# Kernel optimization log

Hardware: AMD Instinct MI355X
Metric: run time of the kernel (lower is better)

## Reference

```python
import jax, jax.numpy as jnp
import numpy as np

B, N, D, H, QK, FF, E, K = 32, 400, 128, 8, 16, 512, 8, 2
LOSS_COEF = 1e-2


def layer_norm(x, g, b, eps=1e-5):
    m = x.mean(-1, keepdims=True)
    v = ((x - m) ** 2).mean(-1, keepdims=True)
    return (x - m) / jnp.sqrt(v + eps) * g + b


def cv_sq(x, eps=1e-10):
    return x.var() / (x.mean() ** 2 + eps)


def setup_inputs() -> dict:
    key = jax.random.key(0)
    ks = jax.random.split(key, 10)
    w = lambda i, shape: jax.random.normal(ks[i], shape, jnp.float32) * 0.02
    return {
        "x": jax.random.normal(ks[0], (B, N, D), jnp.float32),
        "Wq": w(1, (D, H * QK)),
        "Wk": w(2, (D, H * QK)),
        "Wv": w(3, (D, H * QK)),
        "Wo": w(4, (H * QK, D)),
        "bo": jnp.zeros((D,), jnp.float32),
        "ln1_g": jnp.ones((D,), jnp.float32),
        "ln1_b": jnp.zeros((D,), jnp.float32),
        "w_gate": w(5, (D, E)),
        "W1": w(6, (E, D, FF)),
        "b1": jnp.zeros((E, FF), jnp.float32),
        "W2": w(7, (E, FF, D)),
        "b2": jnp.zeros((E, D), jnp.float32),
        "ln2_g": jnp.ones((D,), jnp.float32),
        "ln2_b": jnp.zeros((D,), jnp.float32),
    }


def reference(x, Wq, Wk, Wv, Wo, bo, ln1_g, ln1_b, w_gate, W1, b1, W2, b2, ln2_g, ln2_b):
    b, n, d = x.shape
    # multi-head self-attention (no mask in encoder)
    q = (x @ Wq).reshape(b, n, H, QK).transpose(0, 2, 1, 3)  # [b,h,n,qk]
    k = (x @ Wk).reshape(b, n, H, QK).transpose(0, 2, 1, 3)
    v = (x @ Wv).reshape(b, n, H, QK).transpose(0, 2, 1, 3)
    score = jnp.einsum("bhnd,bhmd->bhnm", q, k) / (QK ** 0.5)
    weights = jax.nn.softmax(score, axis=-1)
    out = jnp.einsum("bhnm,bhmd->bhnd", weights, v)
    out_concat = out.transpose(0, 2, 1, 3).reshape(b, n, H * QK)
    mh = out_concat @ Wo + bo
    out1 = layer_norm(x + mh, ln1_g, ln1_b)

    # MoE feed-forward: noisy top-k gating in eval mode (clean logits)
    xf = out1.reshape(-1, d)                       # [T, D]
    T = xf.shape[0]
    logits = xf @ w_gate                           # [T, E]
    top_vals, top_idx = jax.lax.top_k(logits, K)   # [T, K]
    top_gates = jax.nn.softmax(top_vals, axis=-1)
    gates = jnp.zeros((T, E), xf.dtype).at[jnp.arange(T)[:, None], top_idx].set(top_gates)
    # dense per-expert compute, sparse combine (same math as dispatch/combine)
    h = jax.nn.relu(jnp.einsum("td,edf->etf", xf, W1) + b1[:, None, :])  # [E,T,FF]
    y = jnp.einsum("etf,efd->etd", h, W2) + b2[:, None, :]               # [E,T,D]
    moe_out = jnp.einsum("etd,te->td", y, gates).reshape(b, n, d)
    importance = gates.sum(0)
    load = (gates > 0).sum(0).astype(xf.dtype)
    moe_loss = (cv_sq(importance) + cv_sq(load)) * LOSS_COEF

    out3 = layer_norm(out1 + moe_out, ln2_g, ln2_b)
    return (out3, moe_loss)
```

## Files before the change

kernel.cpp:

```cpp
#include <hip/hip_runtime.h>
#include <hip/hip_bf16.h>
#include <math.h>

#define Bb 32
#define Nn 400
#define Dd 128
#define Hh 8
#define QKd 16
#define FFd 512
#define Ee 8
#define Tt (Bb*Nn)
#define KPAD 434
#define PP2 34

typedef __attribute__((ext_vector_type(8))) __bf16 bf16x8;
typedef __attribute__((ext_vector_type(4))) float f32x4;

#if defined(__has_builtin)
#if __has_builtin(__builtin_amdgcn_exp2f)
#define EXP2(x) __builtin_amdgcn_exp2f(x)
#endif
#endif
#ifndef EXP2
#define EXP2(x) __expf((x) * 0.69314718f)
#endif

__device__ __forceinline__ unsigned short f2bfu(float f){
  union { __hip_bfloat16 h; unsigned short u; } v;
  v.h = __float2bfloat16(f);
  return v.u;
}
__device__ __forceinline__ short f2bf(float f){ return (short)f2bfu(f); }
__device__ __forceinline__ unsigned pack2bf(float a, float b){
  return (unsigned)f2bfu(a) | ((unsigned)f2bfu(b) << 16);
}
__device__ __forceinline__ bf16x8 zero_bf16x8(){
  union { uint4 u; bf16x8 b; } z;
  z.u.x = 0u; z.u.y = 0u; z.u.z = 0u; z.u.w = 0u;
  return z.b;
}

__global__ __launch_bounds__(256) void prep_kernel(
    const float* __restrict__ W1, const float* __restrict__ W2, const float* __restrict__ Wo,
    const float* __restrict__ Wq, const float* __restrict__ Wk, const float* __restrict__ Wv,
    short* __restrict__ W1t, short* __restrict__ W2t, short* __restrict__ wo_t,
    short* __restrict__ qkvw, int* __restrict__ gmeta)
{
  const int bid = blockIdx.x;
  if (bid == 0 && threadIdx.x < 24) gmeta[threadIdx.x] = 0;

  const float* in; short* out; int C, tile;
  if (bid < 512)        { int e = bid >> 6;         tile = bid & 63;          in = W1 + e*65536; out = W1t + e*65536; C = 512; }
  else if (bid < 1024)  { int e = (bid - 512) >> 6; tile = (bid - 512) & 63;  in = W2 + e*65536; out = W2t + e*65536; C = 128; }
  else if (bid < 1040)  { tile = bid - 1024; in = Wo; out = wo_t;          C = 128; }
  else if (bid < 1056)  { tile = bid - 1040; in = Wq; out = qkvw;          C = 128; }
  else if (bid < 1072)  { tile = bid - 1056; in = Wk; out = qkvw + 16384;  C = 128; }
  else                  { tile = bid - 1072; in = Wv; out = qkvw + 32768;  C = 128; }
  const int R = (bid < 512) ? 128 : (bid < 1024 ? 512 : 128);

  __shared__ float t32[32][33];
  const int nCt = C >> 5;
  const int c0 = (tile % nCt) << 5;
  const int r0 = (tile / nCt) << 5;
  const int tx = threadIdx.x & 31, ty = threadIdx.x >> 5;
  #pragma unroll
  for (int i = 0; i < 4; ++i)
    t32[ty + 8*i][tx] = in[(size_t)(r0 + ty + 8*i) * C + c0 + tx];
  __syncthreads();
  #pragma unroll
  for (int i = 0; i < 4; ++i)
    out[(size_t)(c0 + ty + 8*i) * R + r0 + tx] = f2bf(t32[tx][ty + 8*i]);
}

__global__ __launch_bounds__(256) void qkv_kernel(const float* __restrict__ x,
    const short* __restrict__ qkvw,
    short* __restrict__ q, short* __restrict__ k, short* __restrict__ v)
{
  __shared__ short xsh[64][136];
  __shared__ short xsl[64][136];
  const int tid = threadIdx.x;
  const int t0 = blockIdx.x * 64;

  #pragma unroll
  for (int it = 0; it < 8; ++it) {
    int lin = it * 256 + tid;
    int r = lin >> 5;
    int c4 = (lin & 31) << 2;
    float4 xv = *(const float4*)&x[(size_t)(t0 + r) * Dd + c4];
    unsigned h01 = pack2bf(xv.x, xv.y);
    unsigned h23 = pack2bf(xv.z, xv.w);
    union { unsigned u; float f; } ua, ub, uc, ud;
    ua.u = h01 << 16; ub.u = h01 & 0xFFFF0000u;
    uc.u = h23 << 16; ud.u = h23 & 0xFFFF0000u;
    unsigned l01 = pack2bf(xv.x - ua.f, xv.y - ub.f);
    unsigned l23 = pack2bf(xv.z - uc.f, xv.w - ud.f);
    uint2 ph; ph.x = h01; ph.y = h23;
    uint2 pl; pl.x = l01; pl.y = l23;
    *(uint2*)&xsh[r][c4] = ph;
    *(uint2*)&xsl[r][c4] = pl;
  }
  __syncthreads();

  const int lane = tid & 63, w = tid >> 6;
  const int l15 = lane & 15, l4 = lane >> 4;

  f32x4 zero4 = {0.f, 0.f, 0.f, 0.f};
  f32x4 acc[6][4];
  #pragma unroll
  for (int ot = 0; ot < 6; ++ot)
    #pragma unroll
    for (int mt = 0; mt < 4; ++mt) acc[ot][mt] = zero4;

  #pragma unroll
  for (int kt = 0; kt < 4; ++kt) {
    bf16x8 bmh[4], bml[4];
    #pragma unroll
    for (int mt = 0; mt < 4; ++mt) {
      bmh[mt] = *(const bf16x8*)&xsh[mt*16 + l15][kt*32 + l4*8];
      bml[mt] = *(const bf16x8*)&xsl[mt*16 + l15][kt*32 + l4*8];
    }
    #pragma unroll
    for (int ot = 0; ot < 6; ++ot) {
      bf16x8 a = *(const bf16x8*)&qkvw[(size_t)(w*96 + ot*16 + l15) * Dd + kt*32 + l4*8];
      #pragma unroll
      for (int mt = 0; mt < 4; ++mt) {
        acc[ot][mt] = __builtin_amdgcn_mfma_f32_16x16x32_bf16(a, bmh[mt], acc[ot][mt], 0, 0, 0);
        acc[ot][mt] = __builtin_amdgcn_mfma_f32_16x16x32_bf16(a, bml[mt], acc[ot][mt], 0, 0, 0);
      }
    }
  }

  #pragma unroll
  for (int ot = 0; ot < 6; ++ot) {
    const int ob = w*96 + ot*16;
    const int sel = ob >> 7;
    const int hz = (ob & 127) >> 4;
    #pragma unroll
    for (int mt = 0; mt < 4; ++mt) {
      int t = t0 + mt*16 + l15;
      int b = t / Nn, n = t - b * Nn;
      size_t bhn = (size_t)(b*Hh + hz) * Nn + n;
      f32x4 a = acc[ot][mt];
      uint2 p;
      if (sel == 0) {
        p.x = pack2bf(a[0]*0.36067376f, a[1]*0.36067376f);
        p.y = pack2bf(a[2]*0.36067376f, a[3]*0.36067376f);
        *(uint2*)&q[bhn*16 + l4*4] = p;
      } else if (sel == 1) {
        p.x = pack2bf(a[0], a[1]);
        p.y = pack2bf(a[2], a[3]);
        *(uint2*)&k[bhn*16 + l4*4] = p;
      } else {
        p.x = pack2bf(a[0], a[1]);
        p.y = pack2bf(a[2], a[3]);
        *(uint2*)&v[bhn*16 + l4*4] = p;
      }
    }
  }
}

__global__ __launch_bounds__(1024) void attn_kernel(const short* __restrict__ q,
    const short* __restrict__ k, const short* __restrict__ v, short* __restrict__ attn_b)
{
  __shared__ short VT[16 * KPAD];
  __shared__ short P[16][4][16 * PP2];
  const int tid = threadIdx.x;
  const int bh = blockIdx.x;

  {
    const unsigned* vg = (const unsigned*)(v + (size_t)bh * 400 * 16);
    #pragma unroll
    for (int it = 0; it < 4; ++it) {
      int lin = it*1024 + tid;
      if (lin < 3200) {
        int key = lin >> 3, dp = lin & 7;
        unsigned pv = vg[key*8 + dp];
        VT[(2*dp)  * KPAD + key] = (short)(pv & 0xffffu);
        VT[(2*dp+1)* KPAD + key] = (short)(pv >> 16);
      }
    }
    if (tid < 256) {
      int d = tid >> 4, key = 400 + (tid & 15);
      VT[d*KPAD + key] = 0;
    }
  }
  __syncthreads();

  const int w = tid >> 6, lane = tid & 63;
  const int l15 = lane & 15, g = lane >> 4;
  const int p = w & 7, hh = w >> 3;
  const int cc0 = hh ? 7 : 0;
  const int cc1 = hh ? 13 : 7;

  f32x4 zero4 = {0.f, 0.f, 0.f, 0.f};
  f32x4 o[4];
  float lsum[4];
  bf16x8 qf[4];
  #pragma unroll
  for (int i = 0; i < 4; ++i) {
    o[i] = zero4; lsum[i] = 0.f;
    int qt = p + 8*i;
    if (qt < 25 && g < 2)
      qf[i] = *(const bf16x8*)&q[((size_t)bh*400 + qt*16 + l15)*16 + 8*g];
    else
      qf[i] = zero_bf16x8();
  }

  for (int cc = cc0; cc < cc1; ++cc) {
    #pragma unroll
    for (int sub = 0; sub < 2; ++sub) {
      const int kt = cc*2 + sub;
      if (kt < 25) {
        bf16x8 kf;
        if (g < 2) kf = *(const bf16x8*)&k[((size_t)bh*400 + kt*16 + l15)*16 + 8*g];
        else       kf = zero_bf16x8();
        #pragma unroll
        for (int i = 0; i < 4; ++i) {
          int qt = p + 8*i;
          if (qt < 25) {
            f32x4 s = __builtin_amdgcn_mfma_f32_16x16x32_bf16(kf, qf[i], zero4, 0, 0, 0);
            float p0 = EXP2(s[0]);
            float p1 = EXP2(s[1]);
            float p2 = EXP2(s[2]);
            float p3 = EXP2(s[3]);
            lsum[i] += (p0 + p1) + (p2 + p3);
            uint2 pk;
            pk.x = pack2bf(p0, p1);
            pk.y = pack2bf(p2, p3);
            *(uint2*)&P[w][i][l15*PP2 + sub*16 + 4*g] = pk;
          }
        }
      } else {
        uint2 z; z.x = 0u; z.y = 0u;
        #pragma unroll
        for (int i = 0; i < 4; ++i) {
          int qt = p + 8*i;
          if (qt < 25) *(uint2*)&P[w][i][l15*PP2 + sub*16 + 4*g] = z;
        }
      }
    }
    bf16x8 vf = *(const bf16x8*)&VT[l15*KPAD + cc*32 + 8*g];
    #pragma unroll
    for (int i = 0; i < 4; ++i) {
      int qt = p + 8*i;
      if (qt < 25) {
        bf16x8 pf = *(const bf16x8*)&P[w][i][l15*PP2 + 8*g];
        o[i] = __builtin_amdgcn_mfma_f32_16x16x32_bf16(vf, pf, o[i], 0, 0, 0);
      }
    }
  }

  #pragma unroll
  for (int i = 0; i < 4; ++i) {
    lsum[i] += __shfl_xor(lsum[i], 16, 64);
    lsum[i] += __shfl_xor(lsum[i], 32, 64);
  }

  __syncthreads();
  float* CB = (float*)&P[0][0][0];
  if (hh == 1) {
    #pragma unroll
    for (int i = 0; i < 4; ++i) {
      int qt = p + 8*i;
      if (qt < 25) {
        int base = (((p*4) + i)*64 + lane)*5;
        CB[base+0] = o[i][0]; CB[base+1] = o[i][1];
        CB[base+2] = o[i][2]; CB[base+3] = o[i][3];
        CB[base+4] = lsum[i];
      }
    }
  }
  __syncthreads();
  if (hh == 0) {
    const int b = bh >> 3, h = bh & 7;
    #pragma unroll
    for (int i = 0; i < 4; ++i) {
      int qt = p + 8*i;
      if (qt < 25) {
        int base = (((p*4) + i)*64 + lane)*5;
        float o0 = o[i][0] + CB[base+0];
        float o1 = o[i][1] + CB[base+1];
        float o2 = o[i][2] + CB[base+2];
        float o3 = o[i][3] + CB[base+3];
        float ls = lsum[i] + CB[base+4];
        float inv = 1.f / ls;
        uint2 pk;
        pk.x = pack2bf(o0*inv, o1*inv);
        pk.y = pack2bf(o2*inv, o3*inv);
        *(uint2*)&attn_b[((size_t)b*Nn + qt*16 + l15)*Dd + h*16 + 4*g] = pk;
      }
    }
  }
}

__global__ __launch_bounds__(256) void proj_ln1_gate_kernel(
    const float* __restrict__ x, const short* __restrict__ attn_b,
    const short* __restrict__ wo_t, const float* __restrict__ bo,
    const float* __restrict__ g1, const float* __restrict__ b1n,
    const float* __restrict__ w_gate,
    short* __restrict__ out1b,
    int* __restrict__ cnt, float* __restrict__ imp, float* __restrict__ loadv,
    int* __restrict__ etok, float* __restrict__ egate)
{
  __shared__ short as_[64][136];
  __shared__ float reds[4][64];
  __shared__ float reds2[4][64];
  __shared__ float mv[64][2];
  __shared__ float lgs[64*8];
  __shared__ float wgs[128*8];
  __shared__ float s_imp[8], s_load[8];
  __shared__ int s_cnt[8], s_base[8];

  const int tid = threadIdx.x;
  const int t0 = blockIdx.x * 64;

  #pragma unroll
  for (int it = 0; it < 8; ++it) {
    int lin = it * 256 + tid;
    int r = lin >> 5;
    int c4 = (lin & 31) << 2;
    *(uint2*)&as_[r][c4] = *(const uint2*)&attn_b[(size_t)(t0 + r) * Dd + c4];
  }
  #pragma unroll
  for (int it = 0; it < 4; ++it) wgs[it*256 + tid] = w_gate[it*256 + tid];
  lgs[tid] = 0.f; lgs[tid + 256] = 0.f;
  if (tid < 8) { s_imp[tid] = 0.f; s_load[tid] = 0.f; s_cnt[tid] = 0; }
  __syncthreads();

  const int lane = tid & 63, w = tid >> 6;
  const int l15 = lane & 15, l4 = lane >> 4;

  f32x4 zero4 = {0.f, 0.f, 0.f, 0.f};
  f32x4 y[2][4];
  #pragma unroll
  for (int dt = 0; dt < 2; ++dt)
    #pragma unroll
    for (int mt = 0; mt < 4; ++mt) y[dt][mt] = zero4;

  #pragma unroll
  for (int kt = 0; kt < 4; ++kt) {
    bf16x8 a0 = *(const bf16x8*)&wo_t[(size_t)(w*32 + l15) * Dd + kt*32 + l4*8];
    bf16x8 a1 = *(const bf16x8*)&wo_t[(size_t)(w*32 + 16 + l15) * Dd + kt*32 + l4*8];
    bf16x8 bm[4];
    #pragma unroll
    for (int mt = 0; mt < 4; ++mt)
      bm[mt] = *(const bf16x8*)&as_[mt*16 + l15][kt*32 + l4*8];
    #pragma unroll
    for (int mt = 0; mt < 4; ++mt) {
      y[0][mt] = __builtin_amdgcn_mfma_f32_16x16x32_bf16(a0, bm[mt], y[0][mt], 0, 0, 0);
      y[1][mt] = __builtin_amdgcn_mfma_f32_16x16x32_bf16(a1, bm[mt], y[1][mt], 0, 0, 0);
    }
  }

  float4 bov[2];
  bov[0] = *(const float4*)&bo[w*32 + 0*16 + l4*4];
  bov[1] = *(const float4*)&bo[w*32 + 1*16 + l4*4];
  float sP[4], s2P[4];
  #pragma unroll
  for (int mt = 0; mt < 4; ++mt) { sP[mt] = 0.f; s2P[mt] = 0.f; }
  #pragma unroll
  for (int mt = 0; mt < 4; ++mt) {
    int row = mt*16 + l15;
    #pragma unroll
    for (int dt = 0; dt < 2; ++dt) {
      int dim = w*32 + dt*16 + l4*4;
      float4 xv = *(const float4*)&x[(size_t)(t0 + row) * Dd + dim];
      float4 bv = bov[dt];
      f32x4 r = y[dt][mt];
      r[0] += bv.x + xv.x; r[1] += bv.y + xv.y;
      r[2] += bv.z + xv.z; r[3] += bv.w + xv.w;
      y[dt][mt] = r;
      sP[mt]  += (r[0] + r[1]) + (r[2] + r[3]);
      s2P[mt] += (r[0]*r[0] + r[1]*r[1]) + (r[2]*r[2] + r[3]*r[3]);
    }
  }
  #pragma unroll
  for (int mt = 0; mt < 4; ++mt) {
    sP[mt]  += __shfl_xor(sP[mt], 16, 64);  sP[mt]  += __shfl_xor(sP[mt], 32, 64);
    s2P[mt] += __shfl_xor(s2P[mt], 16, 64); s2P[mt] += __shfl_xor(s2P[mt], 32, 64);
  }
  if (l4 == 0) {
    #pragma unroll
    for (int mt = 0; mt < 4; ++mt) {
      reds[w][mt*16 + l15] = sP[mt];
      reds2[w][mt*16 + l15] = s2P[mt];
    }
  }
  __syncthreads();
  if (tid < 64) {
    float s = reds[0][tid] + reds[1][tid] + reds[2][tid] + reds[3][tid];
    float s2 = reds2[0][tid] + reds2[1][tid] + reds2[2][tid] + reds2[3][tid];
    float m = s * (1.f/128.f);
    float var = s2 * (1.f/128.f) - m*m;
    mv[tid][0] = m;
    mv[tid][1] = rsqrtf(var + 1e-5f);
  }
  __syncthreads();

  float4 gv[2], bv2[2];
  #pragma unroll
  for (int dt = 0; dt < 2; ++dt) {
    gv[dt]  = *(const float4*)&g1[w*32 + dt*16 + l4*4];
    bv2[dt] = *(const float4*)&b1n[w*32 + dt*16 + l4*4];
  }
  #pragma unroll
  for (int mt = 0; mt < 4; ++mt) {
    int row = mt*16 + l15;
    float m = mv[row][0], inv = mv[row][1];
    float lg[8];
    #pragma unroll
    for (int e = 0; e < 8; ++e) lg[e] = 0.f;
    #pragma unroll
    for (int dt = 0; dt < 2; ++dt) {
      int dim = w*32 + dt*16 + l4*4;
      f32x4 r = y[dt][mt];
      float o0 = (r[0]-m)*inv*((float*)&gv[dt])[0] + ((float*)&bv2[dt])[0];
      float o1 = (r[1]-m)*inv*((float*)&gv[dt])[1] + ((float*)&bv2[dt])[1];
      float o2 = (r[2]-m)*inv*((float*)&gv[dt])[2] + ((float*)&bv2[dt])[2];
      float o3 = (r[3]-m)*inv*((float*)&gv[dt])[3] + ((float*)&bv2[dt])[3];
      uint2 p; p.x = pack2bf(o0, o1); p.y = pack2bf(o2, o3);
      *(uint2*)&out1b[(size_t)(t0 + row) * Dd + dim] = p;
      #pragma unroll
      for (int e = 0; e < 8; ++e)
        lg[e] += o0*wgs[(dim+0)*8+e] + o1*wgs[(dim+1)*8+e]
               + o2*wgs[(dim+2)*8+e] + o3*wgs[(dim+3)*8+e];
    }
    #pragma unroll
    for (int e = 0; e < 8; ++e) {
      lg[e] += __shfl_xor(lg[e], 16, 64);
      lg[e] += __shfl_xor(lg[e], 32, 64);
    }
    if (l4 == 0) {
      #pragma unroll
      for (int e = 0; e < 8; ++e) atomicAdd(&lgs[row*8 + e], lg[e]);
    }
  }
  __syncthreads();

  int i0 = 0, i1 = -1, p0 = 0, p1 = 0;
  float g0 = 0.f, gg1 = 0.f;
  if (tid < 64) {
    float lgv[8];
    #pragma unroll
    for (int e = 0; e < 8; ++e) lgv[e] = lgs[tid*8 + e];
    float v0 = lgv[0];
    #pragma unroll
    for (int e = 1; e < 8; ++e) if (lgv[e] > v0) { v0 = lgv[e]; i0 = e; }
    float v1 = -INFINITY;
    #pragma unroll
    for (int e = 0; e < 8; ++e) if (e != i0 && lgv[e] > v1) { v1 = lgv[e]; i1 = e; }
    g0 = 1.f / (1.f + __expf(v1 - v0));
    gg1 = 1.f - g0;
    atomicAdd(&s_imp[i0], g0);  atomicAdd(&s_imp[i1], gg1);
    atomicAdd(&s_load[i0], 1.f); atomicAdd(&s_load[i1], 1.f);
    p0 = atomicAdd(&s_cnt[i0], 1);
    p1 = atomicAdd(&s_cnt[i1], 1);
  }
  __syncthreads();
  if (tid < 8) {
    s_base[tid] = atomicAdd(&cnt[tid], s_cnt[tid]);
    atomicAdd(&imp[tid], s_imp[tid]);
    atomicAdd(&loadv[tid], s_load[tid]);
  }
  __syncthreads();
  if (tid < 64) {
    int t = t0 + tid;
    int o0 = i0 * Tt + s_base[i0] + p0;
    etok[o0] = t;               egate[o0] = g0;
    int o1 = i1 * Tt + s_base[i1] + p1;
    etok[o1] = t | (1 << 30);   egate[o1] = gg1;
  }
}

__global__ __launch_bounds__(256) void moe_kernel(const short* __restrict__ out1b,
    const short* __restrict__ W1t, const float* __restrict__ b1,
    const short* __restrict__ W2t, const float* __restrict__ b2,
    const int* __restrict__ cnt, const int* __restrict__ etok, const float* __restrict__ egate,
    short* __restrict__ moe0, short* __restrict__ moe1)
{
  __shared__ short xs[64][136];
  __shared__ short hs[64][136];
  __shared__ int els[64];
  __shared__ float gls[64];

  const int e = blockIdx.y;
  const int count = cnt[e];
  const int t0 = blockIdx.x * 64;
  if (t0 >= count) return;
  const int nt = min(64, count - t0);
  const int tid = threadIdx.x;

  if (tid < 64) {
    int idx = (tid < nt) ? tid : 0;
    els[tid] = etok[e * Tt + t0 + idx];
    gls[tid] = (tid < nt) ? egate[e * Tt + t0 + tid] : 0.f;
  }
  __syncthreads();

  #pragma unroll
  for (int it = 0; it < 8; ++it) {
    int lin = it * 256 + tid;
    int r = lin >> 5;
    int c4 = (lin & 31) << 2;
    int tok = els[r] & 0x3FFFFFFF;
    *(uint2*)&xs[r][c4] = *(const uint2*)&out1b[(size_t)tok * Dd + c4];
  }
  __syncthreads();

  const int lane = tid & 63;
  const int w = tid >> 6;
  const int l15 = lane & 15;
  const int l4 = lane >> 4;

  f32x4 zero4 = {0.f, 0.f, 0.f, 0.f};
  f32x4 y[2][4];
  #pragma unroll
  for (int dt = 0; dt < 2; ++dt)
    #pragma unroll
    for (int mt = 0; mt < 4; ++mt) y[dt][mt] = zero4;

  const short* W1p = W1t + (size_t)e * FFd * Dd;
  const short* W2p = W2t + (size_t)e * Dd * FFd;

  for (int ch = 0; ch < 4; ++ch) {
    f32x4 h[2][4];
    #pragma unroll
    for (int ft = 0; ft < 2; ++ft)
      #pragma unroll
      for (int mt = 0; mt < 4; ++mt) h[ft][mt] = zero4;

    #pragma unroll
    for (int kt = 0; kt < 4; ++kt) {
      bf16x8 a0 = *(const bf16x8*)&W1p[(size_t)(ch*128 + w*32 + 0*16 + l15) * Dd + kt*32 + l4*8];
      bf16x8 a1 = *(const bf16x8*)&W1p[(size_t)(ch*128 + w*32 + 1*16 + l15) * Dd + kt*32 + l4*8];
      bf16x8 bm[4];
      #pragma unroll
      for (int mt = 0; mt < 4; ++mt)
        bm[mt] = *(const bf16x8*)&xs[mt*16 + l15][kt*32 + l4*8];
      #pragma unroll
      for (int mt = 0; mt < 4; ++mt) {
        h[0][mt] = __builtin_amdgcn_mfma_f32_16x16x32_bf16(a0, bm[mt], h[0][mt], 0, 0, 0);
        h[1][mt] = __builtin_amdgcn_mfma_f32_16x16x32_bf16(a1, bm[mt], h[1][mt], 0, 0, 0);
      }
    }

    float4 b1v0 = *(const float4*)&b1[e*FFd + ch*128 + w*32 + 0*16 + l4*4];
    float4 b1v1 = *(const float4*)&b1[e*FFd + ch*128 + w*32 + 1*16 + l4*4];
    __syncthreads();
    #pragma unroll
    for (int mt = 0; mt < 4; ++mt) {
      uint2 p0, p1;
      p0.x = pack2bf(fmaxf(h[0][mt][0] + b1v0.x, 0.f), fmaxf(h[0][mt][1] + b1v0.y, 0.f));
      p0.y = pack2bf(fmaxf(h[0][mt][2] + b1v0.z, 0.f), fmaxf(h[0][mt][3] + b1v0.w, 0.f));
      *(uint2*)&hs[mt*16 + l15][w*32 + 0*16 + l4*4] = p0;
      p1.x = pack2bf(fmaxf(h[1][mt][0] + b1v1.x, 0.f), fmaxf(h[1][mt][1] + b1v1.y, 0.f));
      p1.y = pack2bf(fmaxf(h[1][mt][2] + b1v1.z, 0.f), fmaxf(h[1][mt][3] + b1v1.w, 0.f));
      *(uint2*)&hs[mt*16 + l15][w*32 + 1*16 + l4*4] = p1;
    }
    __syncthreads();

    #pragma unroll
    for (int kt = 0; kt < 4; ++kt) {
      bf16x8 a0 = *(const bf16x8*)&W2p[(size_t)(w*32 + 0*16 + l15) * FFd + ch*128 + kt*32 + l4*8];
      bf16x8 a1 = *(const bf16x8*)&W2p[(size_t)(w*32 + 1*16 + l15) * FFd + ch*128 + kt*32 + l4*8];
      bf16x8 bm[4];
      #pragma unroll
      for (int mt = 0; mt < 4; ++mt)
        bm[mt] = *(const bf16x8*)&hs[mt*16 + l15][kt*32 + l4*8];
      #pragma unroll
      for (int mt = 0; mt < 4; ++mt) {
        y[0][mt] = __builtin_amdgcn_mfma_f32_16x16x32_bf16(a0, bm[mt], y[0][mt], 0, 0, 0);
        y[1][mt] = __builtin_amdgcn_mfma_f32_16x16x32_bf16(a1, bm[mt], y[1][mt], 0, 0, 0);
      }
    }
  }

  float4 b2v[2];
  b2v[0] = *(const float4*)&b2[e*Dd + w*32 + 0*16 + l4*4];
  b2v[1] = *(const float4*)&b2[e*Dd + w*32 + 1*16 + l4*4];
  #pragma unroll
  for (int mt = 0; mt < 4; ++mt) {
    int m = mt*16 + l15;
    if (m < nt) {
      int raw = els[m];
      int t = raw & 0x3FFFFFFF;
      float g = gls[m];
      short* basep = (raw & (1 << 30)) ? moe1 : moe0;
      #pragma unroll
      for (int dt = 0; dt < 2; ++dt) {
        float v0 = g * (y[dt][mt][0] + ((dt == 0) ? b2v[0].x : b2v[1].x));
        float v1 = g * (y[dt][mt][1] + ((dt == 0) ? b2v[0].y : b2v[1].y));
        float v2 = g * (y[dt][mt][2] + ((dt == 0) ? b2v[0].z : b2v[1].z));
        float v3 = g * (y[dt][mt][3] + ((dt == 0) ? b2v[0].w : b2v[1].w));
        uint2 p; p.x = pack2bf(v0, v1); p.y = pack2bf(v2, v3);
        *(uint2*)&basep[(size_t)t * Dd + w*32 + dt*16 + l4*4] = p;
      }
    }
  }
}

__global__ __launch_bounds__(256) void ln2_kernel(const short* __restrict__ out1b,
    const short* __restrict__ moe0, const short* __restrict__ moe1,
    const float* __restrict__ g, const float* __restrict__ bb,
    const float* __restrict__ imp, const float* __restrict__ loadv,
    float* __restrict__ out, float* __restrict__ out_loss)
{
  const int tid = threadIdx.x;
  const int lane = tid & 63;
  const int t = blockIdx.x * 4 + (tid >> 6);
  const int j = lane * 2;

  unsigned xo = *(const unsigned*)&out1b[(size_t)t * Dd + j];
  unsigned m0 = *(const unsigned*)&moe0[(size_t)t * Dd + j];
  unsigned m1 = *(const unsigned*)&moe1[(size_t)t * Dd + j];
  union { unsigned u; float f; } xa, xb, a, b, c, d;
  xa.u = xo << 16; xb.u = xo & 0xFFFF0000u;
  a.u = m0 << 16; b.u = m0 & 0xFFFF0000u;
  c.u = m1 << 16; d.u = m1 & 0xFFFF0000u;
  float r0 = xa.f + a.f + c.f;
  float r1 = xb.f + b.f + d.f;

  float s = r0 + r1;
  float s2 = r0*r0 + r1*r1;
  #pragma unroll
  for (int off = 32; off > 0; off >>= 1) {
    s  += __shfl_xor(s, off, 64);
    s2 += __shfl_xor(s2, off, 64);
  }
  float mean = s * (1.f/128.f);
  float var = s2 * (1.f/128.f) - mean*mean;
  float inv = rsqrtf(var + 1e-5f);
  float2 ov;
  ov.x = (r0 - mean) * inv * g[j]   + bb[j];
  ov.y = (r1 - mean) * inv * g[j+1] + bb[j+1];
  *(float2*)&out[(size_t)t * Dd + j] = ov;

  if (blockIdx.x == 0 && tid == 0) {
    float m1s = 0.f;
    for (int e = 0; e < 8; ++e) m1s += imp[e];
    m1s *= 0.125f;
    float v1 = 0.f;
    for (int e = 0; e < 8; ++e) { float dd = imp[e] - m1s; v1 += dd * dd; }
    v1 *= 0.125f;
    float c1 = v1 / (m1s * m1s + 1e-10f);
    float m2 = 0.f;
    for (int e = 0; e < 8; ++e) m2 += loadv[e];
    m2 *= 0.125f;
    float v2 = 0.f;
    for (int e = 0; e < 8; ++e) { float dd = loadv[e] - m2; v2 += dd * dd; }
    v2 *= 0.125f;
    float c2 = v2 / (m2 * m2 + 1e-10f);
    out_loss[0] = (c1 + c2) * 0.01f;
  }
}

extern "C" void kernel_launch(void* const* d_in, const int* in_sizes, int n_in,
                              void* d_out, int out_size, void* d_ws, size_t ws_size,
                              hipStream_t stream)
{
  (void)in_sizes; (void)n_in; (void)out_size; (void)ws_size;
  const float* x      = (const float*)d_in[0];
  const float* Wq     = (const float*)d_in[1];
  const float* Wk     = (const float*)d_in[2];
  const float* Wv     = (const float*)d_in[3];
  const float* Wo     = (const float*)d_in[4];
  const float* bo     = (const float*)d_in[5];
  const float* ln1_g  = (const float*)d_in[6];
  const float* ln1_b  = (const float*)d_in[7];
  const float* w_gate = (const float*)d_in[8];
  const float* W1     = (const float*)d_in[9];
  const float* b1     = (const float*)d_in[10];
  const float* W2     = (const float*)d_in[11];
  const float* b2     = (const float*)d_in[12];
  const float* ln2_g  = (const float*)d_in[13];
  const float* ln2_b  = (const float*)d_in[14];

  char* wsb = (char*)d_ws;
  size_t off = 0;
  short* attn_b  = (short*)(wsb + off); off += (size_t)Tt*Dd*2;
  short* out1b   = (short*)(wsb + off); off += (size_t)Tt*Dd*2;
  short* moe0    = (short*)(wsb + off); off += (size_t)Tt*Dd*2;
  short* moe1    = (short*)(wsb + off); off += (size_t)Tt*Dd*2;
  short* q_bf    = (short*)(wsb + off); off += (size_t)256*400*16*2;
  short* k_bf    = (short*)(wsb + off); off += (size_t)256*400*16*2;
  short* v_bf    = (short*)(wsb + off); off += (size_t)256*400*16*2;
  short* W1t     = (short*)(wsb + off); off += (size_t)Ee*FFd*Dd*2;
  short* W2t     = (short*)(wsb + off); off += (size_t)Ee*FFd*Dd*2;
  short* wo_t    = (short*)(wsb + off); off += (size_t)Dd*Dd*2;
  short* qkvw    = (short*)(wsb + off); off += (size_t)384*Dd*2;
  int*   gmeta   = (int*)(wsb + off);   off += 256;
  int*   etok    = (int*)(wsb + off);   off += (size_t)Ee*Tt*4;
  float* egate   = (float*)(wsb + off); off += (size_t)Ee*Tt*4;

  int*   cnt   = gmeta;
  float* imp   = (float*)(gmeta + 8);
  float* loadv = (float*)(gmeta + 16);

  float* out3 = (float*)d_out;
  float* loss = out3 + Tt * Dd;

  prep_kernel<<<1088, 256, 0, stream>>>(W1, W2, Wo, Wq, Wk, Wv, W1t, W2t, wo_t, qkvw, gmeta);
  qkv_kernel<<<200, 256, 0, stream>>>(x, qkvw, q_bf, k_bf, v_bf);
  attn_kernel<<<256, 1024, 0, stream>>>(q_bf, k_bf, v_bf, attn_b);
  proj_ln1_gate_kernel<<<200, 256, 0, stream>>>(x, attn_b, wo_t, bo, ln1_g, ln1_b, w_gate,
                                                out1b, cnt, imp, loadv, etok, egate);
  moe_kernel<<<dim3(200, 8), 256, 0, stream>>>(out1b, W1t, b1, W2t, b2, cnt, etok, egate, moe0, moe1);
  ln2_kernel<<<3200, 256, 0, stream>>>(out1b, moe0, moe1, ln2_g, ln2_b, imp, loadv, out3, loss);
}
```

Measured before the change: 96.22 us.

## Double threads per block in qkv and MoE kernels with split-K FF reduction

The qkv kernel now uses 512 threads, each wave computing half as many output tiles. The MoE kernel also goes to 512 threads, splitting the FF dimension into two groups of four waves. Each group keeps its own hidden buffer, and the partial outputs are combined through shared memory before the gated bf16 store. The aim is more waves per block to hide MFMA and load latency, at the cost of more shared memory, an extra reduction step and extra barriers.

```diff
diff --git a/kernel.cpp b/kernel.cpp
--- a/kernel.cpp
+++ b/kernel.cpp
@@ -72,7 +72,7 @@
     out[(size_t)(c0 + ty + 8*i) * R + r0 + tx] = f2bf(t32[tx][ty + 8*i]);
 }
 
-__global__ __launch_bounds__(256) void qkv_kernel(const float* __restrict__ x,
+__global__ __launch_bounds__(512) void qkv_kernel(const float* __restrict__ x,
     const short* __restrict__ qkvw,
     short* __restrict__ q, short* __restrict__ k, short* __restrict__ v)
 {
@@ -82,8 +82,8 @@
   const int t0 = blockIdx.x * 64;
 
   #pragma unroll
-  for (int it = 0; it < 8; ++it) {
-    int lin = it * 256 + tid;
+  for (int it = 0; it < 4; ++it) {
+    int lin = it * 512 + tid;
     int r = lin >> 5;
     int c4 = (lin & 31) << 2;
     float4 xv = *(const float4*)&x[(size_t)(t0 + r) * Dd + c4];
@@ -105,9 +105,9 @@
   const int l15 = lane & 15, l4 = lane >> 4;
 
   f32x4 zero4 = {0.f, 0.f, 0.f, 0.f};
-  f32x4 acc[6][4];
-  #pragma unroll
-  for (int ot = 0; ot < 6; ++ot)
+  f32x4 acc[3][4];
+  #pragma unroll
+  for (int ot = 0; ot < 3; ++ot)
     #pragma unroll
     for (int mt = 0; mt < 4; ++mt) acc[ot][mt] = zero4;
 
@@ -120,8 +120,8 @@
       bml[mt] = *(const bf16x8*)&xsl[mt*16 + l15][kt*32 + l4*8];
     }
     #pragma unroll
-    for (int ot = 0; ot < 6; ++ot) {
-      bf16x8 a = *(const bf16x8*)&qkvw[(size_t)(w*96 + ot*16 + l15) * Dd + kt*32 + l4*8];
+    for (int ot = 0; ot < 3; ++ot) {
+      bf16x8 a = *(const bf16x8*)&qkvw[(size_t)(w*48 + ot*16 + l15) * Dd + kt*32 + l4*8];
       #pragma unroll
       for (int mt = 0; mt < 4; ++mt) {
         acc[ot][mt] = __builtin_amdgcn_mfma_f32_16x16x32_bf16(a, bmh[mt], acc[ot][mt], 0, 0, 0);
@@ -131,8 +131,8 @@
   }
 
   #pragma unroll
-  for (int ot = 0; ot < 6; ++ot) {
-    const int ob = w*96 + ot*16;
+  for (int ot = 0; ot < 3; ++ot) {
+    const int ob = w*48 + ot*16;
     const int sel = ob >> 7;
     const int hz = (ob & 127) >> 4;
     #pragma unroll
@@ -472,14 +472,18 @@
   }
 }
 
-__global__ __launch_bounds__(256) void moe_kernel(const short* __restrict__ out1b,
+union MoeShared {
+  struct { short xs[64][136]; short hs[2][64][136]; } s;
+  float comb[4][64][36];
+};
+
+__global__ __launch_bounds__(512) void moe_kernel(const short* __restrict__ out1b,
     const short* __restrict__ W1t, const float* __restrict__ b1,
     const short* __restrict__ W2t, const float* __restrict__ b2,
     const int* __restrict__ cnt, const int* __restrict__ etok, const float* __restrict__ egate,
     short* __restrict__ moe0, short* __restrict__ moe1)
 {
-  __shared__ short xs[64][136];
-  __shared__ short hs[64][136];
+  __shared__ MoeShared su;
   __shared__ int els[64];
   __shared__ float gls[64];
 
@@ -498,17 +502,19 @@
   __syncthreads();
 
   #pragma unroll
-  for (int it = 0; it < 8; ++it) {
-    int lin = it * 256 + tid;
+  for (int it = 0; it < 4; ++it) {
+    int lin = it * 512 + tid;
     int r = lin >> 5;
     int c4 = (lin & 31) << 2;
     int tok = els[r] & 0x3FFFFFFF;
-    *(uint2*)&xs[r][c4] = *(const uint2*)&out1b[(size_t)tok * Dd + c4];
+    *(uint2*)&su.s.xs[r][c4] = *(const uint2*)&out1b[(size_t)tok * Dd + c4];
   }
   __syncthreads();
 
   const int lane = tid & 63;
   const int w = tid >> 6;
+  const int grp = w >> 2;
+  const int wp = w & 3;
   const int l15 = lane & 15;
   const int l4 = lane >> 4;
 
@@ -521,8 +527,11 @@
 
   const short* W1p = W1t + (size_t)e * FFd * Dd;
   const short* W2p = W2t + (size_t)e * Dd * FFd;
-
-  for (int ch = 0; ch < 4; ++ch) {
+  short (*hsg)[136] = su.s.hs[grp];
+
+  #pragma unroll
+  for (int c = 0; c < 2; ++c) {
+    const int ch = grp*2 + c;
     f32x4 h[2][4];
     #pragma unroll
     for (int ft = 0; ft < 2; ++ft)
@@ -531,12 +540,12 @@
 
     #pragma unroll
     for (int kt = 0; kt < 4; ++kt) {
-      bf16x8 a0 = *(const bf16x8*)&W1p[(size_t)(ch*128 + w*32 + 0*16 + l15) * Dd + kt*32 + l4*8];
-      bf16x8 a1 = *(const bf16x8*)&W1p[(size_t)(ch*128 + w*32 + 1*16 + l15) * Dd + kt*32 + l4*8];
+      bf16x8 a0 = *(const bf16x8*)&W1p[(size_t)(ch*128 + wp*32 + 0*16 + l15) * Dd + kt*32 + l4*8];
+      bf16x8 a1 = *(const bf16x8*)&W1p[(size_t)(ch*128 + wp*32 + 1*16 + l15) * Dd + kt*32 + l4*8];
       bf16x8 bm[4];
       #pragma unroll
       for (int mt = 0; mt < 4; ++mt)
-        bm[mt] = *(const bf16x8*)&xs[mt*16 + l15][kt*32 + l4*8];
+        bm[mt] = *(const bf16x8*)&su.s.xs[mt*16 + l15][kt*32 + l4*8];
       #pragma unroll
       for (int mt = 0; mt < 4; ++mt) {
         h[0][mt] = __builtin_amdgcn_mfma_f32_16x16x32_bf16(a0, bm[mt], h[0][mt], 0, 0, 0);
@@ -544,29 +553,29 @@
       }
     }
 
-    float4 b1v0 = *(const float4*)&b1[e*FFd + ch*128 + w*32 + 0*16 + l4*4];
-    float4 b1v1 = *(const float4*)&b1[e*FFd + ch*128 + w*32 + 1*16 + l4*4];
+    float4 b1v0 = *(const float4*)&b1[e*FFd + ch*128 + wp*32 + 0*16 + l4*4];
+    float4 b1v1 = *(const float4*)&b1[e*FFd + ch*128 + wp*32 + 1*16 + l4*4];
     __syncthreads();
     #pragma unroll
     for (int mt = 0; mt < 4; ++mt) {
       uint2 p0, p1;
       p0.x = pack2bf(fmaxf(h[0][mt][0] + b1v0.x, 0.f), fmaxf(h[0][mt][1] + b1v0.y, 0.f));
       p0.y = pack2bf(fmaxf(h[0][mt][2] + b1v0.z, 0.f), fmaxf(h[0][mt][3] + b1v0.w, 0.f));
-      *(uint2*)&hs[mt*16 + l15][w*32 + 0*16 + l4*4] = p0;
+      *(uint2*)&hsg[mt*16 + l15][wp*32 + 0*16 + l4*4] = p0;
       p1.x = pack2bf(fmaxf(h[1][mt][0] + b1v1.x, 0.f), fmaxf(h[1][mt][1] + b1v1.y, 0.f));
       p1.y = pack2bf(fmaxf(h[1][mt][2] + b1v1.z, 0.f), fmaxf(h[1][mt][3] + b1v1.w, 0.f));
-      *(uint2*)&hs[mt*16 + l15][w*32 + 1*16 + l4*4] = p1;
+      *(uint2*)&hsg[mt*16 + l15][wp*32 + 1*16 + l4*4] = p1;
     }
     __syncthreads();
 
     #pragma unroll
     for (int kt = 0; kt < 4; ++kt) {
-      bf16x8 a0 = *(const bf16x8*)&W2p[(size_t)(w*32 + 0*16 + l15) * FFd + ch*128 + kt*32 + l4*8];
-      bf16x8 a1 = *(const bf16x8*)&W2p[(size_t)(w*32 + 1*16 + l15) * FFd + ch*128 + kt*32 + l4*8];
+      bf16x8 a0 = *(const bf16x8*)&W2p[(size_t)(wp*32 + 0*16 + l15) * FFd + ch*128 + kt*32 + l4*8];
+      bf16x8 a1 = *(const bf16x8*)&W2p[(size_t)(wp*32 + 1*16 + l15) * FFd + ch*128 + kt*32 + l4*8];
       bf16x8 bm[4];
       #pragma unroll
       for (int mt = 0; mt < 4; ++mt)
-        bm[mt] = *(const bf16x8*)&hs[mt*16 + l15][kt*32 + l4*8];
+        bm[mt] = *(const bf16x8*)&hsg[mt*16 + l15][kt*32 + l4*8];
       #pragma unroll
       for (int mt = 0; mt < 4; ++mt) {
         y[0][mt] = __builtin_amdgcn_mfma_f32_16x16x32_bf16(a0, bm[mt], y[0][mt], 0, 0, 0);
@@ -575,25 +584,43 @@
     }
   }
 
-  float4 b2v[2];
-  b2v[0] = *(const float4*)&b2[e*Dd + w*32 + 0*16 + l4*4];
-  b2v[1] = *(const float4*)&b2[e*Dd + w*32 + 1*16 + l4*4];
-  #pragma unroll
-  for (int mt = 0; mt < 4; ++mt) {
-    int m = mt*16 + l15;
-    if (m < nt) {
-      int raw = els[m];
-      int t = raw & 0x3FFFFFFF;
-      float g = gls[m];
-      short* basep = (raw & (1 << 30)) ? moe1 : moe0;
-      #pragma unroll
-      for (int dt = 0; dt < 2; ++dt) {
-        float v0 = g * (y[dt][mt][0] + ((dt == 0) ? b2v[0].x : b2v[1].x));
-        float v1 = g * (y[dt][mt][1] + ((dt == 0) ? b2v[0].y : b2v[1].y));
-        float v2 = g * (y[dt][mt][2] + ((dt == 0) ? b2v[0].z : b2v[1].z));
-        float v3 = g * (y[dt][mt][3] + ((dt == 0) ? b2v[0].w : b2v[1].w));
-        uint2 p; p.x = pack2bf(v0, v1); p.y = pack2bf(v2, v3);
-        *(uint2*)&basep[(size_t)t * Dd + w*32 + dt*16 + l4*4] = p;
+  __syncthreads();
+  if (grp == 1) {
+    float* cb = &su.comb[wp][lane][0];
+    #pragma unroll
+    for (int dt = 0; dt < 2; ++dt)
+      #pragma unroll
+      for (int mt = 0; mt < 4; ++mt) {
+        float4 v4;
+        v4.x = y[dt][mt][0]; v4.y = y[dt][mt][1];
+        v4.z = y[dt][mt][2]; v4.w = y[dt][mt][3];
+        *(float4*)&cb[(dt*4+mt)*4] = v4;
+      }
+  }
+  __syncthreads();
+  if (grp == 0) {
+    const float* cb = &su.comb[wp][lane][0];
+    float4 b2v[2];
+    b2v[0] = *(const float4*)&b2[e*Dd + wp*32 + 0*16 + l4*4];
+    b2v[1] = *(const float4*)&b2[e*Dd + wp*32 + 1*16 + l4*4];
+    #pragma unroll
+    for (int mt = 0; mt < 4; ++mt) {
+      int m = mt*16 + l15;
+      if (m < nt) {
+        int raw = els[m];
+        int t = raw & 0x3FFFFFFF;
+        float g = gls[m];
+        short* basep = (raw & (1 << 30)) ? moe1 : moe0;
+        #pragma unroll
+        for (int dt = 0; dt < 2; ++dt) {
+          float4 yo = *(const float4*)&cb[(dt*4+mt)*4];
+          float v0 = g * (y[dt][mt][0] + yo.x + ((dt == 0) ? b2v[0].x : b2v[1].x));
+          float v1 = g * (y[dt][mt][1] + yo.y + ((dt == 0) ? b2v[0].y : b2v[1].y));
+          float v2 = g * (y[dt][mt][2] + yo.z + ((dt == 0) ? b2v[0].z : b2v[1].z));
+          float v3 = g * (y[dt][mt][3] + yo.w + ((dt == 0) ? b2v[0].w : b2v[1].w));
+          uint2 p; p.x = pack2bf(v0, v1); p.y = pack2bf(v2, v3);
+          *(uint2*)&basep[(size_t)t * Dd + wp*32 + dt*16 + l4*4] = p;
+        }
       }
     }
   }
@@ -700,10 +727,10 @@
   float* loss = out3 + Tt * Dd;
 
   prep_kernel<<<1088, 256, 0, stream>>>(W1, W2, Wo, Wq, Wk, Wv, W1t, W2t, wo_t, qkvw, gmeta);
-  qkv_kernel<<<200, 256, 0, stream>>>(x, qkvw, q_bf, k_bf, v_bf);
+  qkv_kernel<<<200, 512, 0, stream>>>(x, qkvw, q_bf, k_bf, v_bf);
   attn_kernel<<<256, 1024, 0, stream>>>(q_bf, k_bf, v_bf, attn_b);
   proj_ln1_gate_kernel<<<200, 256, 0, stream>>>(x, attn_b, wo_t, bo, ln1_g, ln1_b, w_gate,
                                                 out1b, cnt, imp, loadv, etok, egate);
-  moe_kernel<<<dim3(200, 8), 256, 0, stream>>>(out1b, W1t, b1, W2t, b2, cnt, etok, egate, moe0, moe1);
+  moe_kernel<<<dim3(200, 8), 512, 0, stream>>>(out1b, W1t, b1, W2t, b2, cnt, etok, egate, moe0, moe1);
   ln2_kernel<<<3200, 256, 0, stream>>>(out1b, moe0, moe1, ln2_g, ln2_b, imp, loadv, out3, loss);
 }
```

New measurement: 78.49 us (median of 2 runs). -18.4%, faster.
